# Optimization experiments

Hardware: AMD Instinct MI355X
Metric: run time of the kernel (lower is better)

Reference implementation:

```python
import jax, jax.numpy as jnp
import numpy as np

SIZE = 7  # grid size; H = W = SIZE


def setup_inputs() -> dict:
    key = jax.random.key(0)
    k1, k2, k3, k4 = jax.random.split(key, 4)
    N, C = 256, 2048
    x = jax.random.normal(k1, (N, C, SIZE, SIZE), dtype=jnp.float32)
    mask = jax.random.uniform(k2, (N, SIZE, SIZE), dtype=jnp.float32)
    W = jax.random.normal(k3, (2, 2 * C), dtype=jnp.float32) * 0.02
    b = jax.random.normal(k4, (2,), dtype=jnp.float32) * 0.02
    return {"x": x, "mask": mask, "W": W, "b": b}


def reference(x, mask, W, b):
    N, C, H, Wd = x.shape
    HW = H * Wd
    size = float(H)
    # (N, HW, C) tokens
    reduced_x = jnp.transpose(x.reshape(N, C, HW), (0, 2, 1))
    m = mask.reshape(N, HW)
    thr = jnp.mean(m, axis=1, keepdims=True)  # curr_coef = 1.0
    binary_mask = (m > thr).astype(x.dtype)  # (N, HW)
    # mean over channels of masked tokens, then argmax over positions
    masked_mean = jnp.mean(reduced_x * binary_mask[:, :, None], axis=-1)  # (N, HW)
    max_index = jnp.argmax(masked_mean, axis=-1)  # (N,)
    batch_idx = jnp.arange(N)
    max_features = reduced_x[batch_idx, max_index]  # (N, C)
    # concat(max_feature, token) -> tiny linear 2C -> 2 with ReLU
    disc = jnp.concatenate(
        [jnp.broadcast_to(max_features[:, None, :], (N, HW, C)), reduced_x], axis=-1
    )  # (N, HW, 2C)
    preds_coord = jax.nn.relu(jnp.einsum('npc,oc->npo', disc, W) + b)  # (N, HW, 2)
    # zero out prediction at the anchor position
    preds_coord = preds_coord.at[batch_idx, max_index].set(0.0)
    # polar-coordinate targets relative to anchor
    ii, jj = jnp.meshgrid(jnp.arange(H), jnp.arange(Wd), indexing='ij')
    label = jnp.stack([ii, jj], axis=-1).astype(x.dtype).reshape(HW, 2)  # (HW, 2)
    basic_anchor = label[max_index][:, None, :]  # (N, 1, 2)
    rel = (label[None, :, :] - basic_anchor) / size  # (N, HW, 2)
    relative_dist = jnp.sqrt(jnp.sum(rel ** 2, axis=-1))  # (N, HW)
    relative_angle = jnp.arctan2(rel[:, :, 1], rel[:, :, 0])
    relative_angle = (relative_angle / jnp.float32(np.pi) + 1.0) / 2.0  # (N, HW)
    preds_dist = preds_coord[:, :, 0]
    preds_angle = preds_coord[:, :, 1]
    dist_loss = (preds_dist - relative_dist) ** 2
    gap = preds_angle - relative_angle
    gap = jnp.where(gap < 0, gap + 1.0, gap)
    gap = gap - jnp.mean(gap, axis=-1, keepdims=True)
    angle_loss = gap ** 2
    return (dist_loss + angle_loss).reshape(N, H, Wd)
```

## Files before the change

kernel.cpp:

```cpp
#include <hip/hip_runtime.h>
#include <math.h>

#define N_     256
#define C_     2048
#define HW_    49
#define CHUNKS 8
#define CPB    (C_/CHUNKS)
#define TILE_C 64
#define NG     5

__global__ __launch_bounds__(256) void k_reduce(const float* __restrict__ x,
                                                const float* __restrict__ Wm,
                                                float* __restrict__ part) {
  const int chunk = blockIdx.x;
  const int n     = blockIdx.y;
  const int t     = threadIdx.x;

  __shared__ float4 tile4[(TILE_C*HW_)/4];
  __shared__ float  wt[NG][TILE_C];
  float* tile = (float*)tile4;

  const int g = t / HW_;
  const int p = t - g*HW_;

  float acc = 0.f;

  for (int tc = 0; tc < CPB; tc += TILE_C) {
    const int c0 = chunk*CPB + tc;
    const float4* src = (const float4*)(x + ((size_t)n*C_ + (size_t)c0)*HW_);
    #pragma unroll
    for (int i = 0; i < 4; ++i) {
      int idx = t + i*256;
      if (idx < (TILE_C*HW_)/4) tile4[idx] = src[idx];
    }
    for (int i = t; i < NG*TILE_C; i += 256) {
      int gg = i / TILE_C, cc = i - gg*TILE_C;
      float w;
      if (gg == 0) w = 1.f;
      else {
        int row  = (gg-1) & 1;
        int half = (gg-1) >> 1;
        w = Wm[row*(2*C_) + half*C_ + c0 + cc];
      }
      wt[gg][cc] = w;
    }
    __syncthreads();
    if (g < NG) {
      #pragma unroll 8
      for (int c = 0; c < TILE_C; ++c)
        acc = fmaf(tile[c*HW_ + p], wt[g][c], acc);
    }
    __syncthreads();
  }
  if (g < NG)
    part[((size_t)n*CHUNKS + chunk)*(NG*HW_) + t] = acc;
}

__global__ __launch_bounds__(256) void k_final(const float* __restrict__ part,
                                               const float* __restrict__ mask,
                                               const float* __restrict__ b,
                                               float* __restrict__ out) {
  const int n = blockIdx.x;
  const int t = threadIdx.x;
  __shared__ float red[NG*HW_];

  if (t < NG*HW_) {
    float a = 0.f;
    #pragma unroll
    for (int ch = 0; ch < CHUNKS; ++ch)
      a += part[((size_t)n*CHUNKS + ch)*(NG*HW_) + t];
    red[t] = a;
  }
  __syncthreads();

  if (t < 64) {
    const int  p   = t;
    const bool act = (p < HW_);

    float m = act ? mask[n*HW_ + p] : 0.f;
    float tot = m;
    #pragma unroll
    for (int off = 32; off; off >>= 1) tot += __shfl_xor(tot, off);
    const float thr = tot / 49.f;

    float s  = act ? red[0*HW_ + p] : 0.f;
    float mm = act ? ((m > thr) ? (s * (1.f/2048.f)) : 0.f) : -INFINITY;
    float best = mm;
    int   bidx = act ? p : 64;
    #pragma unroll
    for (int off = 32; off; off >>= 1) {
      float ov = __shfl_xor(best, off);
      int   oi = __shfl_xor(bidx, off);
      if (ov > best || (ov == best && oi < bidx)) { best = ov; bidx = oi; }
    }
    const int mi = bidx;

    const float u0mi = red[1*HW_ + mi];
    const float u1mi = red[2*HW_ + mi];

    float pred0 = 0.f, pred1 = 0.f;
    if (act) {
      pred0 = fmaxf(u0mi + red[3*HW_ + p] + b[0], 0.f);
      pred1 = fmaxf(u1mi + red[4*HW_ + p] + b[1], 0.f);
      if (p == mi) { pred0 = 0.f; pred1 = 0.f; }
    }

    const int ii = p / 7,  jj = p - ii*7;
    const int ai = mi / 7, aj = mi - ai*7;
    const float ri = (float)(ii - ai) / 7.f;
    const float rj = (float)(jj - aj) / 7.f;
    const float dist = sqrtf(ri*ri + rj*rj);
    const float ang  = (atan2f(rj, ri) / 3.14159274101257324f + 1.f) * 0.5f;

    float gap = pred1 - ang;
    if (gap < 0.f) gap += 1.f;
    float gsum = act ? gap : 0.f;
    #pragma unroll
    for (int off = 32; off; off >>= 1) gsum += __shfl_xor(gsum, off);
    const float gmean = gsum / 49.f;

    if (act) {
      const float dl = pred0 - dist;
      const float ga = gap - gmean;
      out[n*HW_ + p] = dl*dl + ga*ga;
    }
  }
}

extern "C" void kernel_launch(void* const* d_in, const int* in_sizes, int n_in,
                              void* d_out, int out_size, void* d_ws, size_t ws_size,
                              hipStream_t stream) {
  const float* x    = (const float*)d_in[0];
  const float* mask = (const float*)d_in[1];
  const float* Wm   = (const float*)d_in[2];
  const float* b    = (const float*)d_in[3];
  float* out  = (float*)d_out;
  float* part = (float*)d_ws;

  dim3 g1(CHUNKS, N_);
  k_reduce<<<g1, 256, 0, stream>>>(x, Wm, part);
  k_final<<<N_, 256, 0, stream>>>(part, mask, b, out);
}
```

Measured before the change: 161.7 us.

## Replace LDS-tiled reduction with per-wave register accumulation of five dot products

The reduction kernel no longer stages x and W tiles through shared memory. Each wavefront now owns a contiguous channel range: every lane reads one spatial position per channel and keeps five accumulators in registers (the channel sum plus four W dot products), and the four waves are combined through a small shared buffer at the end. The chunk count is halved, so there are fewer blocks and fewer partial rows for the final kernel to add. The aim is to drop the repeated __syncthreads and LDS traffic and to compute all five outputs from a single read of x, but the global reads become scalar loads of 49 floats per row (15 of 64 lanes idle) instead of float4 loads, which may coalesce less well.

```diff
diff --git a/kernel.cpp b/kernel.cpp
--- a/kernel.cpp
+++ b/kernel.cpp
@@ -4,56 +4,55 @@
 #define N_     256
 #define C_     2048
 #define HW_    49
-#define CHUNKS 8
+#define CHUNKS 4
 #define CPB    (C_/CHUNKS)
-#define TILE_C 64
+#define CPW    (CPB/4)
 #define NG     5
 
-__global__ __launch_bounds__(256) void k_reduce(const float* __restrict__ x,
-                                                const float* __restrict__ Wm,
-                                                float* __restrict__ part) {
+__global__ __launch_bounds__(256) void k_dot(const float* __restrict__ x,
+                                             const float* __restrict__ Wm,
+                                             float* __restrict__ part) {
   const int chunk = blockIdx.x;
   const int n     = blockIdx.y;
   const int t     = threadIdx.x;
+  const int w     = t >> 6;
+  const int l     = t & 63;
 
-  __shared__ float4 tile4[(TILE_C*HW_)/4];
-  __shared__ float  wt[NG][TILE_C];
-  float* tile = (float*)tile4;
+  __shared__ float red[4][NG][HW_ + 7];
 
-  const int g = t / HW_;
-  const int p = t - g*HW_;
+  const int cbase = chunk*CPB + w*CPW;
+  const float* xq   = x + ((size_t)n*C_ + cbase)*HW_ + (l < HW_ ? l : 0);
+  const float* w_u0 = Wm + cbase;
+  const float* w_u1 = Wm + 2*C_ + cbase;
+  const float* w_t0 = Wm + C_ + cbase;
+  const float* w_t1 = Wm + 3*C_ + cbase;
 
-  float acc = 0.f;
+  float a0=0.f, a1=0.f, a2=0.f, a3=0.f, a4=0.f;
+  #pragma unroll 8
+  for (int c = 0; c < CPW; ++c) {
+    const float xv = xq[(size_t)c*HW_];
+    const float b0 = w_u0[c];
+    const float b1 = w_u1[c];
+    const float b2 = w_t0[c];
+    const float b3 = w_t1[c];
+    a0 += xv;
+    a1 = fmaf(xv, b0, a1);
+    a2 = fmaf(xv, b1, a2);
+    a3 = fmaf(xv, b2, a3);
+    a4 = fmaf(xv, b3, a4);
+  }
 
-  for (int tc = 0; tc < CPB; tc += TILE_C) {
-    const int c0 = chunk*CPB + tc;
-    const float4* src = (const float4*)(x + ((size_t)n*C_ + (size_t)c0)*HW_);
-    #pragma unroll
-    for (int i = 0; i < 4; ++i) {
-      int idx = t + i*256;
-      if (idx < (TILE_C*HW_)/4) tile4[idx] = src[idx];
-    }
-    for (int i = t; i < NG*TILE_C; i += 256) {
-      int gg = i / TILE_C, cc = i - gg*TILE_C;
-      float w;
-      if (gg == 0) w = 1.f;
-      else {
-        int row  = (gg-1) & 1;
-        int half = (gg-1) >> 1;
-        w = Wm[row*(2*C_) + half*C_ + c0 + cc];
-      }
-      wt[gg][cc] = w;
-    }
-    __syncthreads();
-    if (g < NG) {
-      #pragma unroll 8
-      for (int c = 0; c < TILE_C; ++c)
-        acc = fmaf(tile[c*HW_ + p], wt[g][c], acc);
-    }
-    __syncthreads();
+  if (l < HW_) {
+    red[w][0][l] = a0; red[w][1][l] = a1; red[w][2][l] = a2;
+    red[w][3][l] = a3; red[w][4][l] = a4;
   }
-  if (g < NG)
-    part[((size_t)n*CHUNKS + chunk)*(NG*HW_) + t] = acc;
+  __syncthreads();
+
+  if (t < NG*HW_) {
+    const int g = t / HW_, p = t - g*HW_;
+    const float s = red[0][g][p] + red[1][g][p] + red[2][g][p] + red[3][g][p];
+    part[((size_t)n*CHUNKS + chunk)*(NG*HW_) + t] = s;
+  }
 }
 
 __global__ __launch_bounds__(256) void k_final(const float* __restrict__ part,
@@ -138,6 +137,6 @@
   float* part = (float*)d_ws;
 
   dim3 g1(CHUNKS, N_);
-  k_reduce<<<g1, 256, 0, stream>>>(x, Wm, part);
+  k_dot<<<g1, 256, 0, stream>>>(x, Wm, part);
   k_final<<<N_, 256, 0, stream>>>(part, mask, b, out);
 }
```

Measured after the change: 167.3 us. +3.5%, slower.
